# Kernel optimization log

Measured on AMD Instinct MI355X. Metric: run time of the kernel, lower is better.

The kernel has to match this reference:

```python
import jax, jax.numpy as jnp
import numpy as np

EPS = 1e-16

def setup_inputs() -> dict:
    key = jax.random.key(0)
    u = jax.random.normal(key, (16, 1024, 1024, 1), dtype=jnp.float32)
    return {"u": u}

def reference(u) -> jnp.ndarray:
    # Reflect-pad H and W by 1 (matches tf.pad mode='REFLECT').
    p = jnp.pad(u, ((0, 0), (1, 1), (1, 1), (0, 0)), mode='reflect')
    c = p[:, 1:-1, 1:-1, :]  # center = u
    # The six 3x3 'convs' are shift-subtract stencils (TF conv = correlation):
    dxf = p[:, 2:, 1:-1, :] - c                          # dxforward:  u[i+1,j]-u[i,j]
    dxb = c - p[:, :-2, 1:-1, :]                         # dxback:     u[i,j]-u[i-1,j]
    dyf = p[:, 1:-1, 2:, :] - c                          # dyforward:  u[i,j+1]-u[i,j]
    dyb = c - p[:, 1:-1, :-2, :]                         # dybackward: u[i,j]-u[i,j-1]
    dsbf = p[:, :-2, 2:, :] - p[:, :-2, 1:-1, :]         # dystepbackforward
    dslf = p[:, 2:, :-2, :] - p[:, 1:-1, :-2, :]         # dxstepleftforward
    F = jnp.sqrt(dxf * dxf + dyf * dyf + EPS)
    G = jnp.sqrt(dxb * dxb + dsbf * dsbf + EPS)
    H = jnp.sqrt(dslf * dslf + dyb * dyb + EPS)
    return dxf / F - dxb / G + dyf / F - dyb / H
```

## Files before the change

kernel.cpp:

```cpp
#include <hip/hip_runtime.h>
#include <hip/hip_bf16.h>


#define Wdim 1024
#define Hdim 1024
#define EPSf 1e-16f
#define TR 8

typedef float v4f __attribute__((ext_vector_type(4)));

__global__ __launch_bounds__(256) void curv_kernel(const float* __restrict__ u,
                                                   float* __restrict__ out) {
    int blk = ((blockIdx.x & 7) << 8) | (blockIdx.x >> 3);
    int q  = threadIdx.x;
    int w0 = q << 2;
    int rowBlk = blk & 127;
    int b      = blk >> 7;
    int r0     = rowBlk << 3;

    const float* base = u + ((size_t)b << 20);

    int rIdx[TR + 2];
    rIdx[0] = (r0 == 0) ? 1 : r0 - 1;
#pragma unroll
    for (int k = 1; k <= TR; ++k) rIdx[k] = r0 + k - 1;
    rIdx[TR + 1] = (r0 + TR == Hdim) ? Hdim - 2 : r0 + TR;

    v4f R[TR + 2];
#pragma unroll
    for (int k = 0; k < TR + 2; ++k)
        R[k] = ((const v4f*)(base + (size_t)rIdx[k] * Wdim))[q];

    float Lv[TR + 2], Rv[TR + 2];
#pragma unroll
    for (int k = 1; k < TR + 2; ++k) Lv[k] = __shfl_up(R[k].w, 1);
#pragma unroll
    for (int k = 0; k < TR + 1; ++k) Rv[k] = __shfl_down(R[k].x, 1);

    int lane = threadIdx.x & 63;
    if (lane == 0) {
        if (w0 == 0) {
#pragma unroll
            for (int k = 1; k < TR + 2; ++k) Lv[k] = R[k].y;
        } else {
#pragma unroll
            for (int k = 1; k < TR + 2; ++k)
                Lv[k] = base[(size_t)rIdx[k] * Wdim + w0 - 1];
        }
    }
    if (lane == 63) {
        if (w0 + 4 == Wdim) {
#pragma unroll
            for (int k = 0; k < TR + 1; ++k) Rv[k] = R[k].z;
        } else {
#pragma unroll
            for (int k = 0; k < TR + 1; ++k)
                Rv[k] = base[(size_t)rIdx[k] * Wdim + w0 + 4];
        }
    }

    size_t obase = ((size_t)b << 20) + (size_t)r0 * Wdim;
#pragma unroll
    for (int j = 0; j < TR; ++j) {
        v4f C = R[1 + j];
        v4f M = R[j];
        v4f P = R[2 + j];
        float c[6] = {Lv[1 + j], C.x, C.y, C.z, C.w, Rv[1 + j]};
        float m[5] = {M.x, M.y, M.z, M.w, Rv[j]};
        float p[5] = {Lv[2 + j], P.x, P.y, P.z, P.w};

        v4f o;
#pragma unroll
        for (int i = 0; i < 4; ++i) {
            float cc   = c[i + 1];
            float cyp  = c[i + 2];
            float cym  = c[i];
            float mm   = m[i];
            float myp  = m[i + 1];
            float pp   = p[i + 1];
            float pym  = p[i];

            float dxf  = pp  - cc;
            float dxb  = cc  - mm;
            float dyf  = cyp - cc;
            float dyb  = cc  - cym;
            float dsbf = myp - mm;
            float dslf = pym - cym;

            float invF = rsqrtf(dxf * dxf + dyf * dyf + EPSf);
            float invG = rsqrtf(dxb * dxb + dsbf * dsbf + EPSf);
            float invH = rsqrtf(dslf * dslf + dyb * dyb + EPSf);

            o[i] = (dxf + dyf) * invF - dxb * invG - dyb * invH;
        }
        __builtin_nontemporal_store(o, (v4f*)(out + obase + (size_t)j * Wdim) + q);
    }
}

extern "C" void kernel_launch(void* const* d_in, const int* in_sizes, int n_in,
                              void* d_out, int out_size, void* d_ws, size_t ws_size,
                              hipStream_t stream) {
    const float* u = (const float*)d_in[0];
    float* out = (float*)d_out;
    curv_kernel<<<2048, 256, 0, stream>>>(u, out);
}
```

Before: 107.7 us.

## Stream rows through a rolling 3-row register window with one-row prefetch

Replaces the up-front load of all ten rows with a rolling window of three rows held in registers. The loop is not unrolled, and each iteration prefetches the next row before computing the current output row. This cuts register pressure, which may raise occupancy. The cost is less memory-level parallelism per thread, since only one row load is in flight at a time, plus serialized shuffles and loop overhead.

```diff
diff --git a/kernel.cpp b/kernel.cpp
--- a/kernel.cpp
+++ b/kernel.cpp
@@ -1,5 +1,4 @@
 #include <hip/hip_runtime.h>
-#include <hip/hip_bf16.h>
 
 
 #define Wdim 1024
@@ -17,57 +16,47 @@
     int rowBlk = blk & 127;
     int b      = blk >> 7;
     int r0     = rowBlk << 3;
+    int lane   = threadIdx.x & 63;
 
     const float* base = u + ((size_t)b << 20);
 
-    int rIdx[TR + 2];
-    rIdx[0] = (r0 == 0) ? 1 : r0 - 1;
-#pragma unroll
-    for (int k = 1; k <= TR; ++k) rIdx[k] = r0 + k - 1;
-    rIdx[TR + 1] = (r0 + TR == Hdim) ? Hdim - 2 : r0 + TR;
+    auto loadrow = [&](int r) -> v4f {
+        return ((const v4f*)(base + (size_t)r * Wdim))[q];
+    };
+    auto edges = [&](v4f R, int r, float& L, float& Rt) {
+        L  = __shfl_up(R.w, 1);
+        Rt = __shfl_down(R.x, 1);
+        if (lane == 0)
+            L = (w0 == 0) ? R.y : base[(size_t)r * Wdim + w0 - 1];
+        if (lane == 63)
+            Rt = (w0 + 4 == Wdim) ? R.z : base[(size_t)r * Wdim + w0 + 4];
+    };
 
-    v4f R[TR + 2];
-#pragma unroll
-    for (int k = 0; k < TR + 2; ++k)
-        R[k] = ((const v4f*)(base + (size_t)rIdx[k] * Wdim))[q];
+    int rm = (r0 == 0) ? 1 : r0 - 1;
+    v4f M = loadrow(rm);
+    v4f C = loadrow(r0);
+    v4f P = loadrow(r0 + 1);
 
-    float Lv[TR + 2], Rv[TR + 2];
-#pragma unroll
-    for (int k = 1; k < TR + 2; ++k) Lv[k] = __shfl_up(R[k].w, 1);
-#pragma unroll
-    for (int k = 0; k < TR + 1; ++k) Rv[k] = __shfl_down(R[k].x, 1);
+    float LvM, RvM, LvC, RvC, LvP, RvP;
+    edges(M, rm,     LvM, RvM);
+    edges(C, r0,     LvC, RvC);
+    edges(P, r0 + 1, LvP, RvP);
 
-    int lane = threadIdx.x & 63;
-    if (lane == 0) {
-        if (w0 == 0) {
-#pragma unroll
-            for (int k = 1; k < TR + 2; ++k) Lv[k] = R[k].y;
-        } else {
-#pragma unroll
-            for (int k = 1; k < TR + 2; ++k)
-                Lv[k] = base[(size_t)rIdx[k] * Wdim + w0 - 1];
+    float* o0 = out + ((size_t)b << 20) + (size_t)r0 * Wdim;
+
+#pragma unroll 1
+    for (int j = 0; j < TR; ++j) {
+        v4f N;
+        int rp = r0 + j + 2;
+        bool pre = (j < TR - 1);
+        if (pre) {
+            if (rp == Hdim) rp = Hdim - 2;
+            N = loadrow(rp);
         }
-    }
-    if (lane == 63) {
-        if (w0 + 4 == Wdim) {
-#pragma unroll
-            for (int k = 0; k < TR + 1; ++k) Rv[k] = R[k].z;
-        } else {
-#pragma unroll
-            for (int k = 0; k < TR + 1; ++k)
-                Rv[k] = base[(size_t)rIdx[k] * Wdim + w0 + 4];
-        }
-    }
 
-    size_t obase = ((size_t)b << 20) + (size_t)r0 * Wdim;
-#pragma unroll
-    for (int j = 0; j < TR; ++j) {
-        v4f C = R[1 + j];
-        v4f M = R[j];
-        v4f P = R[2 + j];
-        float c[6] = {Lv[1 + j], C.x, C.y, C.z, C.w, Rv[1 + j]};
-        float m[5] = {M.x, M.y, M.z, M.w, Rv[j]};
-        float p[5] = {Lv[2 + j], P.x, P.y, P.z, P.w};
+        float c[6] = {LvC, C.x, C.y, C.z, C.w, RvC};
+        float m[5] = {M.x, M.y, M.z, M.w, RvM};
+        float p[5] = {LvP, P.x, P.y, P.z, P.w};
 
         v4f o;
 #pragma unroll
@@ -93,7 +82,15 @@
 
             o[i] = (dxf + dyf) * invF - dxb * invG - dyb * invH;
         }
-        __builtin_nontemporal_store(o, (v4f*)(out + obase + (size_t)j * Wdim) + q);
+        __builtin_nontemporal_store(o, (v4f*)(o0 + (size_t)j * Wdim) + q);
+
+        if (pre) {
+            M = C;  RvM = RvC;
+            C = P;  LvC = LvP; RvC = RvP;
+            float LvN, RvN;
+            edges(N, rp, LvN, RvN);
+            P = N;  LvP = LvN; RvP = RvN;
+        }
     }
 }
 
```

Measured after the change: 112.0 us. 4.0% more time.
